# Optimization experiments

Hardware: AMD Instinct MI355X
Metric: run time of the kernel (lower is better)

## Reference

```python
import jax, jax.numpy as jnp
import numpy as np

KERNELS = (7, 9, 11)   # kernel_sizes, dilation=1 each
HEADS_PER = 2          # num_head // len(kernel_sizes)
HEAD_DIM = 32          # dim // num_head
DIM = 192


def _win_idx(L, K):
    # NATTEN non-causal window start: centered, clamped to stay in-bounds.
    starts = jnp.clip(jnp.arange(L) - K // 2, 0, L - K)
    return starts[:, None] + jnp.arange(K)[None, :]  # [L, K]


def _na2d(q, k, v, K):
    # q,k,v: [B, h, H, W, D]; q pre-scaled. Neighborhood attention, kernel KxK.
    B, h, H, W, D = q.shape
    ih = _win_idx(H, K)  # [H, K]
    iw = _win_idx(W, K)  # [W, K]
    kr = k[:, :, ih]     # [B, h, H, Kh, W, D]  rows gathered once
    # loop over the Kw kernel taps (small fixed structural loop)
    attn = jnp.stack(
        [jnp.einsum('bnijd,bnikjd->bnijk', q, kr[:, :, :, :, iw[:, kw], :])
         for kw in range(K)], axis=-1)                 # [B,h,H,W,Kh,Kw]
    attn = jax.nn.softmax(attn.reshape(B, h, H, W, K * K), axis=-1)
    attn = attn.reshape(B, h, H, W, K, K)
    vr = v[:, :, ih]     # [B, h, H, Kh, W, D]
    y = jnp.zeros_like(q)
    for kw in range(K):
        y = y + jnp.einsum('bnijk,bnikjd->bnijd',
                           attn[..., kw], vr[:, :, :, :, iw[:, kw], :])
    return y             # [B, h, H, W, D]


def _forward(x, w_qkv, b_qkv, w_proj, b_proj):
    B, H, W, C = x.shape
    qkv = x @ w_qkv + b_qkv                      # [B,H,W,3*DIM]
    scale = HEAD_DIM ** -0.5
    outs = []
    off = 0
    for K in KERNELS:
        ch = 3 * HEADS_PER * HEAD_DIM            # 192 per scale
        xi = qkv[..., off:off + ch]
        off += ch
        r = xi.reshape(B, H, W, 3, HEADS_PER, HEAD_DIM)
        q = jnp.transpose(r[:, :, :, 0], (0, 3, 1, 2, 4)) * scale
        k = jnp.transpose(r[:, :, :, 1], (0, 3, 1, 2, 4))
        v = jnp.transpose(r[:, :, :, 2], (0, 3, 1, 2, 4))
        y = _na2d(q, k, v, K)                    # [B,h,H,W,D]
        outs.append(jnp.transpose(y, (0, 2, 3, 1, 4)).reshape(B, H, W, HEADS_PER * HEAD_DIM))
    out = jnp.concatenate(outs, axis=-1)         # [B,H,W,DIM]
    return out @ w_proj + b_proj


def setup_inputs() -> dict:
    key = jax.random.key(0)
    ks = jax.random.split(key, 4)
    x = jax.random.normal(ks[0], (4, 96, 96, DIM), jnp.float32)
    w_qkv = jax.random.normal(ks[1], (DIM, 3 * DIM), jnp.float32) * 0.02
    b_qkv = jnp.zeros((3 * DIM,), jnp.float32)
    w_proj = jax.random.normal(ks[2], (DIM, DIM), jnp.float32) * 0.02
    b_proj = jnp.zeros((DIM,), jnp.float32)
    return {'x': x, 'w_qkv': w_qkv, 'b_qkv': b_qkv, 'w_proj': w_proj, 'b_proj': b_proj}


def reference(x, w_qkv, b_qkv, w_proj, b_proj):
    return _forward(x, w_qkv, b_qkv, w_proj, b_proj)
```

## Files before the change

### kernel.cpp

```cpp
#include <hip/hip_runtime.h>
#include <cstddef>

constexpr int B_ = 4, H_ = 96, W_ = 96, C_ = 192, QKVC = 576;
constexpr int NPIX = B_ * H_ * W_;
constexpr float C2 = 0.25503486208385085f;

typedef __attribute__((ext_vector_type(8))) short bf16x8;
typedef __attribute__((ext_vector_type(4))) float f32x4;
typedef unsigned short ushort_t;

__device__ __forceinline__ unsigned short f2bf(float f) {
    unsigned int u = __builtin_bit_cast(unsigned int, f);
    u += 0x7fffu + ((u >> 16) & 1u);
    return (unsigned short)(u >> 16);
}
__device__ __forceinline__ float bf2f(unsigned short h) {
    unsigned int u = ((unsigned int)h) << 16;
    return __builtin_bit_cast(float, u);
}
__device__ __forceinline__ unsigned int pack2(unsigned short a, unsigned short b) {
    return (unsigned int)a | ((unsigned int)b << 16);
}
__device__ __forceinline__ float fexp2(float x) {
#if __has_builtin(__builtin_amdgcn_exp2f)
    return __builtin_amdgcn_exp2f(x);
#else
    return __expf(x * 0.6931471805599453f);
#endif
}

__global__ __launch_bounds__(256) void convert_x_kernel(
    const float* __restrict__ x, ushort_t* __restrict__ xh, int n4)
{
    int i = blockIdx.x * 256 + threadIdx.x;
    if (i >= n4) return;
    float4 v = ((const float4*)x)[i];
    uint2 p;
    p.x = pack2(f2bf(v.x), f2bf(v.y));
    p.y = pack2(f2bf(v.z), f2bf(v.w));
    ((uint2*)xh)[i] = p;
}

__global__ __launch_bounds__(256) void convert_w_kernel(
    const float* __restrict__ w_qkv, const float* __restrict__ w_proj,
    ushort_t* __restrict__ wqt, ushort_t* __restrict__ wpt_h,
    ushort_t* __restrict__ wpt_l)
{
    int idx = blockIdx.x * 256 + threadIdx.x;
    if (idx < 576 * 192) {
        int n = idx / 192, k = idx - n * 192;
        wqt[idx] = f2bf(w_qkv[(size_t)k * 576 + n]);
    } else {
        int i2 = idx - 576 * 192;
        if (i2 < 192 * 192) {
            int n = i2 / 192, k = i2 - n * 192;
            float v = w_proj[(size_t)k * 192 + n];
            unsigned short h = f2bf(v);
            wpt_h[i2] = h;
            wpt_l[i2] = f2bf(v - bf2f(h));
        }
    }
}

template<bool BSPLIT, bool OUTBF, bool VT, int NT>
__global__ __launch_bounds__(256) void gemm_mfma2_kernel(
    const ushort_t* __restrict__ A,
    const ushort_t* __restrict__ Bt_h, const ushort_t* __restrict__ Bt_l,
    const float* __restrict__ bias, void* __restrict__ Cout,
    ushort_t* __restrict__ vTout, int M, int N, int K)
{
    constexpr int NPB = BSPLIT ? 2 : 1;
    constexpr int NI = NT / 32;
    __shared__ __align__(16) ushort_t As[8 * 64 * 8];
    __shared__ __align__(16) ushort_t Bs[NPB][8 * NT * 8];

    const int tid = threadIdx.x;
    const int lane = tid & 63;
    const int w = tid >> 6;
    const int wm = (w & 1) * 32;
    const int wn = (w >> 1) * (NT / 2);
    const int fm = lane & 15;
    const int fq = lane >> 4;

    const int phys = blockIdx.x;
    const int bid = (phys & 7) * (int)(gridDim.x >> 3) + (phys >> 3);
    const int ntiles = N / NT;
    const int m0 = (bid / ntiles) * 64;
    const int n0 = (bid % ntiles) * NT;

    f32x4 acc[2][NI];
    #pragma unroll
    for (int mi = 0; mi < 2; ++mi)
        #pragma unroll
        for (int ni = 0; ni < NI; ++ni)
            acc[mi][ni] = (f32x4){0.f, 0.f, 0.f, 0.f};

    for (int k0 = 0; k0 < K; k0 += 64) {
        __syncthreads();
        #pragma unroll
        for (int it = 0; it < 2; ++it) {
            int idx = it * 256 + tid;
            int m = idx >> 3, kc = idx & 7;
            uint4 v = *(const uint4*)(A + (size_t)(m0 + m) * K + k0 + kc * 8);
            *(uint4*)(&As[0] + (kc * 64 + (m ^ kc)) * 8) = v;
        }
        #pragma unroll
        for (int it = 0; it < NI; ++it) {
            int idx = it * 256 + tid;
            int n = idx >> 3, kc = idx & 7;
            int phys_g = kc * NT + (n ^ kc);
            *(uint4*)(&Bs[0][0] + phys_g * 8) =
                *(const uint4*)(Bt_h + (size_t)(n0 + n) * K + k0 + kc * 8);
            if constexpr (BSPLIT)
                *(uint4*)(&Bs[NPB - 1][0] + phys_g * 8) =
                    *(const uint4*)(Bt_l + (size_t)(n0 + n) * K + k0 + kc * 8);
        }
        __syncthreads();

        #pragma unroll
        for (int kt2 = 0; kt2 < 2; ++kt2) {
            const int kc = kt2 * 4 + fq;
            bf16x8 ah[2], bh[NI];
            #pragma unroll
            for (int mi = 0; mi < 2; ++mi)
                ah[mi] = *(const bf16x8*)(&As[0] + (kc * 64 + ((wm + mi * 16 + fm) ^ kc)) * 8);
            #pragma unroll
            for (int ni = 0; ni < NI; ++ni)
                bh[ni] = *(const bf16x8*)(&Bs[0][0] + (kc * NT + ((wn + ni * 16 + fm) ^ kc)) * 8);
            #pragma unroll
            for (int mi = 0; mi < 2; ++mi)
                #pragma unroll
                for (int ni = 0; ni < NI; ++ni)
                    acc[mi][ni] = __builtin_amdgcn_mfma_f32_16x16x32_bf16(
                        ah[mi], bh[ni], acc[mi][ni], 0, 0, 0);
            if constexpr (BSPLIT) {
                bf16x8 bl[NI];
                #pragma unroll
                for (int ni = 0; ni < NI; ++ni)
                    bl[ni] = *(const bf16x8*)(&Bs[NPB - 1][0] + (kc * NT + ((wn + ni * 16 + fm) ^ kc)) * 8);
                #pragma unroll
                for (int mi = 0; mi < 2; ++mi)
                    #pragma unroll
                    for (int ni = 0; ni < NI; ++ni)
                        acc[mi][ni] = __builtin_amdgcn_mfma_f32_16x16x32_bf16(
                            ah[mi], bl[ni], acc[mi][ni], 0, 0, 0);
            }
        }
    }

    #pragma unroll
    for (int ni = 0; ni < NI; ++ni) {
        const int lcol = wn + ni * 16 + fm;
        const int col = n0 + lcol;
        const float bv = bias[col];
        const int vl = lcol - 128;
        #pragma unroll
        for (int mi = 0; mi < 2; ++mi) {
            const int rbase = m0 + wm + mi * 16 + fq * 4;
            if constexpr (VT) {
                if (vl >= 0) {
                    int bb = rbase / 9216;
                    int rem = rbase - bb * 9216;
                    int ii = rem / 96;
                    int jj = rem - ii * 96;
                    int hh = vl >> 5, dd = vl & 31;
                    unsigned long long pk =
                          (unsigned long long)f2bf(acc[mi][ni][0] + bv)
                        | ((unsigned long long)f2bf(acc[mi][ni][1] + bv) << 16)
                        | ((unsigned long long)f2bf(acc[mi][ni][2] + bv) << 32)
                        | ((unsigned long long)f2bf(acc[mi][ni][3] + bv) << 48);
                    *(unsigned long long*)(vTout
                        + ((size_t)((bb * 96 + ii) * 6) + (n0 / 192) * 2 + hh) * 3072
                        + (size_t)dd * 96 + jj) = pk;
                    continue;
                }
            }
            #pragma unroll
            for (int r = 0; r < 4; ++r) {
                float val = acc[mi][ni][r] + bv;
                if constexpr (OUTBF)
                    ((ushort_t*)Cout)[(size_t)(rbase + r) * N + col] = f2bf(val);
                else
                    ((float*)Cout)[(size_t)(rbase + r) * N + col] = val;
            }
        }
    }
}

__global__ __launch_bounds__(384, 5) void na2d_kernel(
    const ushort_t* __restrict__ qkv, const ushort_t* __restrict__ vT,
    ushort_t* __restrict__ attn)
{
    __shared__ ushort_t Kb[2][96 * 40];
    __shared__ ushort_t Vtb[2][32 * 104];

    int phys = blockIdx.x;
    int idx = (phys & 7) * 288 + (phys >> 3);

    const int g = idx % 3; idx /= 3;
    const int h = idx & 1; idx >>= 1;
    const int i = idx % 96;
    const int b = idx / 96;

    const int K = 7 + 2 * g, cc = K >> 1;
    int si = i - cc; if (si < 0) si = 0; if (si > H_ - K) si = H_ - K;

    const int tid = threadIdx.x;
    const int w = tid >> 6, lane = tid & 63;
    const int fm = lane & 15, fq = lane >> 4;
    const int pixbase = w * 16;

    int cb = (pixbase - cc) & ~7;
    if (cb < 0) cb = 0; if (cb > 64) cb = 64;
    const int col0 = cb + fm, col1 = cb + 16 + fm;

    const int jlane = pixbase + fm;
    int sjl = jlane - cc; if (sjl < 0) sjl = 0; if (sjl > W_ - K) sjl = W_ - K;
    float b0[4], b1[4];
    #pragma unroll
    for (int r = 0; r < 4; ++r) {
        b0[r] = ((unsigned)(cb + fq * 4 + r - sjl)      < (unsigned)K) ? 0.f : -1e30f;
        b1[r] = ((unsigned)(cb + 16 + fq * 4 + r - sjl) < (unsigned)K) ? 0.f : -1e30f;
    }

    const size_t rowstride = (size_t)W_ * QKVC;
    const bf16x8 qfrag = *(const bf16x8*)(
        qkv + (size_t)(b * H_ + i) * rowstride + (size_t)jlane * QKVC
        + g * 192 + h * 32 + fq * 8);

    const int scol = tid >> 2, sch = tid & 3;
    const size_t kgoff = (size_t)scol * QKVC + g * 192 + 64 + h * 32 + sch * 8;
    const int klds = scol * 40 + ((sch ^ (scol & 3)) << 3);
    const int vd = tid / 12, vc8 = tid - vd * 12;
    const int vlds = vd * 104 + vc8 * 8;
    const size_t vslice = ((size_t)((b * H_ + si) * 6) + g * 2 + h) * 3072;

    f32x4 y0 = {0.f, 0.f, 0.f, 0.f}, y1 = {0.f, 0.f, 0.f, 0.f};
    float lsum = 0.f;

    uint4 kv = *(const uint4*)(qkv + (size_t)(b * H_ + si) * rowstride + kgoff);
    uint4 vv = *(const uint4*)(vT + vslice + (size_t)tid * 8);

    for (int t = 0; t < K; ++t) {
        *(uint4*)&Kb[t & 1][klds] = kv;
        *(uint4*)&Vtb[t & 1][vlds] = vv;
        if (t + 1 < K) {
            kv = *(const uint4*)(qkv + (size_t)(b * H_ + si + t + 1) * rowstride + kgoff);
            vv = *(const uint4*)(vT + vslice + (size_t)(t + 1) * 18432 + (size_t)tid * 8);
        }
        __syncthreads();

        bf16x8 kf0 = *(const bf16x8*)&Kb[t & 1][col0 * 40 + ((fq ^ (col0 & 3)) << 3)];
        bf16x8 kf1 = *(const bf16x8*)&Kb[t & 1][col1 * 40 + ((fq ^ (col1 & 3)) << 3)];
        const ushort_t* vb0 = &Vtb[t & 1][fm * 104 + cb + fq * 4];
        const ushort_t* vb1 = &Vtb[t & 1][(16 + fm) * 104 + cb + fq * 4];
        uint2 va0 = *(const uint2*)(vb0);
        uint2 va1 = *(const uint2*)(vb0 + 16);
        uint2 va2 = *(const uint2*)(vb1);
        uint2 va3 = *(const uint2*)(vb1 + 16);
        const bf16x8 cv0 = __builtin_bit_cast(bf16x8, (uint4){va0.x, va0.y, va1.x, va1.y});
        const bf16x8 cv1 = __builtin_bit_cast(bf16x8, (uint4){va2.x, va2.y, va3.x, va3.y});

        f32x4 s0 = __builtin_amdgcn_mfma_f32_16x16x32_bf16(
            kf0, qfrag, (f32x4){0.f, 0.f, 0.f, 0.f}, 0, 0, 0);
        f32x4 s1 = __builtin_amdgcn_mfma_f32_16x16x32_bf16(
            kf1, qfrag, (f32x4){0.f, 0.f, 0.f, 0.f}, 0, 0, 0);

        unsigned short p00 = f2bf(fexp2(fmaf(s0[0], C2, b0[0])));
        unsigned short p01 = f2bf(fexp2(fmaf(s0[1], C2, b0[1])));
        unsigned short p02 = f2bf(fexp2(fmaf(s0[2], C2, b0[2])));
        unsigned short p03 = f2bf(fexp2(fmaf(s0[3], C2, b0[3])));
        unsigned short p10 = f2bf(fexp2(fmaf(s1[0], C2, b1[0])));
        unsigned short p11 = f2bf(fexp2(fmaf(s1[1], C2, b1[1])));
        unsigned short p12 = f2bf(fexp2(fmaf(s1[2], C2, b1[2])));
        unsigned short p13 = f2bf(fexp2(fmaf(s1[3], C2, b1[3])));
        lsum += (bf2f(p00) + bf2f(p01)) + (bf2f(p02) + bf2f(p03))
              + (bf2f(p10) + bf2f(p11)) + (bf2f(p12) + bf2f(p13));
        const bf16x8 pa = __builtin_bit_cast(bf16x8, (uint4){
            pack2(p00, p01), pack2(p02, p03),
            pack2(p10, p11), pack2(p12, p13)});

        y0 = __builtin_amdgcn_mfma_f32_16x16x32_bf16(pa, cv0, y0, 0, 0, 0);
        y1 = __builtin_amdgcn_mfma_f32_16x16x32_bf16(pa, cv1, y1, 0, 0, 0);
    }

    lsum += __shfl_xor(lsum, 16);
    lsum += __shfl_xor(lsum, 32);

    #pragma unroll
    for (int r = 0; r < 4; ++r) {
        const float l = __shfl(lsum, fq * 4 + r);
        const float inv = 1.f / l;
        const int j = pixbase + fq * 4 + r;
        const size_t o = (size_t)((b * H_ + i) * W_ + j) * C_ + g * 64 + h * 32 + fm;
        attn[o]      = f2bf(y0[r] * inv);
        attn[o + 16] = f2bf(y1[r] * inv);
    }
}

extern "C" void kernel_launch(void* const* d_in, const int* in_sizes, int n_in,
                              void* d_out, int out_size, void* d_ws, size_t ws_size,
                              hipStream_t stream)
{
    const float* x      = (const float*)d_in[0];
    const float* w_qkv  = (const float*)d_in[1];
    const float* b_qkv  = (const float*)d_in[2];
    const float* w_proj = (const float*)d_in[3];
    const float* b_proj = (const float*)d_in[4];
    float* out = (float*)d_out;

    char* ws = (char*)d_ws;
    ushort_t* qkvh  = (ushort_t*)ws;
    char*     reg1  = ws + (size_t)NPIX * QKVC * 2;
    ushort_t* xh    = (ushort_t*)reg1;
    ushort_t* attn  = (ushort_t*)reg1;
    char*     wbase = reg1 + (size_t)NPIX * C_ * 2;
    ushort_t* wqt   = (ushort_t*)wbase;
    ushort_t* wpt_h = (ushort_t*)(wbase + 576 * 192 * 2);
    ushort_t* wpt_l = (ushort_t*)(wbase + 576 * 192 * 2 + 192 * 192 * 2);
    ushort_t* vT    = (ushort_t*)(wbase + 576 * 192 * 2 + 2 * 192 * 192 * 2);

    convert_x_kernel<<<(NPIX * C_ / 4 + 255) / 256, 256, 0, stream>>>(
        x, xh, NPIX * C_ / 4);
    convert_w_kernel<<<(576 * 192 + 192 * 192 + 255) / 256, 256, 0, stream>>>(
        w_qkv, w_proj, wqt, wpt_h, wpt_l);

    gemm_mfma2_kernel<false, true, true, 192><<<(NPIX / 64) * (QKVC / 192), 256, 0, stream>>>(
        xh, wqt, nullptr, b_qkv, qkvh, vT, NPIX, QKVC, C_);

    na2d_kernel<<<2304, 384, 0, stream>>>(qkvh, vT, attn);

    gemm_mfma2_kernel<true, false, false, 96><<<(NPIX / 64) * (C_ / 96), 256, 0, stream>>>(
        attn, wpt_h, wpt_l, b_proj, out, nullptr, NPIX, C_, C_);
}
```

Measured before the change: 155.5 us.

## Fuse x fp32-to-bf16 conversion into QKV GEMM and register-prefetch next K tile

The separate kernel that converts x to bf16 is removed. The QKV GEMM now reads fp32 x directly and packs it to bf16 while writing shared memory, which saves one launch and a full write and re-read of a bf16 copy of x. The GEMM main loop is also restructured so the next K tile's global loads are issued into registers before the MFMA work on the current tile, overlapping memory latency with compute. In exchange the kernel uses more registers, and the QKV GEMM reads twice as many A bytes because x is now fp32. Since x is converted three times (once per N tile), the fp32 reads are repeated.

```diff
diff --git a/kernel.cpp b/kernel.cpp
--- a/kernel.cpp
+++ b/kernel.cpp
@@ -27,18 +27,6 @@
 #else
     return __expf(x * 0.6931471805599453f);
 #endif
-}
-
-__global__ __launch_bounds__(256) void convert_x_kernel(
-    const float* __restrict__ x, ushort_t* __restrict__ xh, int n4)
-{
-    int i = blockIdx.x * 256 + threadIdx.x;
-    if (i >= n4) return;
-    float4 v = ((const float4*)x)[i];
-    uint2 p;
-    p.x = pack2(f2bf(v.x), f2bf(v.y));
-    p.y = pack2(f2bf(v.z), f2bf(v.w));
-    ((uint2*)xh)[i] = p;
 }
 
 __global__ __launch_bounds__(256) void convert_w_kernel(
@@ -62,9 +50,9 @@
     }
 }
 
-template<bool BSPLIT, bool OUTBF, bool VT, int NT>
+template<bool BSPLIT, bool OUTBF, bool VT, int NT, bool AF32>
 __global__ __launch_bounds__(256) void gemm_mfma2_kernel(
-    const ushort_t* __restrict__ A,
+    const void* __restrict__ Ain,
     const ushort_t* __restrict__ Bt_h, const ushort_t* __restrict__ Bt_l,
     const float* __restrict__ bias, void* __restrict__ Cout,
     ushort_t* __restrict__ vTout, int M, int N, int K)
@@ -88,6 +76,9 @@
     const int m0 = (bid / ntiles) * 64;
     const int n0 = (bid % ntiles) * NT;
 
+    const int sa_m  = (tid >> 3);
+    const int sa_kc = tid & 7;
+
     f32x4 acc[2][NI];
     #pragma unroll
     for (int mi = 0; mi < 2; ++mi)
@@ -95,26 +86,63 @@
         for (int ni = 0; ni < NI; ++ni)
             acc[mi][ni] = (f32x4){0.f, 0.f, 0.f, 0.f};
 
-    for (int k0 = 0; k0 < K; k0 += 64) {
-        __syncthreads();
+    float4 af[2][2];
+    uint4  au[2];
+    uint4  bu[NI];
+    uint4  blu[BSPLIT ? NI : 1];
+
+    const int NS = K / 64;
+
+    auto stage = [&](int k0) {
         #pragma unroll
         for (int it = 0; it < 2; ++it) {
-            int idx = it * 256 + tid;
-            int m = idx >> 3, kc = idx & 7;
-            uint4 v = *(const uint4*)(A + (size_t)(m0 + m) * K + k0 + kc * 8);
-            *(uint4*)(&As[0] + (kc * 64 + (m ^ kc)) * 8) = v;
+            const int m = sa_m + it * 32;
+            if constexpr (AF32) {
+                const float* ap = (const float*)Ain + (size_t)(m0 + m) * K + k0 + sa_kc * 8;
+                af[it][0] = *(const float4*)(ap);
+                af[it][1] = *(const float4*)(ap + 4);
+            } else {
+                au[it] = *(const uint4*)((const ushort_t*)Ain
+                    + (size_t)(m0 + m) * K + k0 + sa_kc * 8);
+            }
         }
         #pragma unroll
         for (int it = 0; it < NI; ++it) {
-            int idx = it * 256 + tid;
-            int n = idx >> 3, kc = idx & 7;
-            int phys_g = kc * NT + (n ^ kc);
-            *(uint4*)(&Bs[0][0] + phys_g * 8) =
-                *(const uint4*)(Bt_h + (size_t)(n0 + n) * K + k0 + kc * 8);
+            const int n = sa_m + it * 32;
+            bu[it] = *(const uint4*)(Bt_h + (size_t)(n0 + n) * K + k0 + sa_kc * 8);
             if constexpr (BSPLIT)
-                *(uint4*)(&Bs[NPB - 1][0] + phys_g * 8) =
-                    *(const uint4*)(Bt_l + (size_t)(n0 + n) * K + k0 + kc * 8);
-        }
+                blu[it] = *(const uint4*)(Bt_l + (size_t)(n0 + n) * K + k0 + sa_kc * 8);
+        }
+    };
+    auto commit = [&]() {
+        #pragma unroll
+        for (int it = 0; it < 2; ++it) {
+            const int m = sa_m + it * 32;
+            uint4 v;
+            if constexpr (AF32) {
+                v.x = pack2(f2bf(af[it][0].x), f2bf(af[it][0].y));
+                v.y = pack2(f2bf(af[it][0].z), f2bf(af[it][0].w));
+                v.z = pack2(f2bf(af[it][1].x), f2bf(af[it][1].y));
+                v.w = pack2(f2bf(af[it][1].z), f2bf(af[it][1].w));
+            } else {
+                v = au[it];
+            }
+            *(uint4*)(&As[0] + (sa_kc * 64 + (m ^ sa_kc)) * 8) = v;
+        }
+        #pragma unroll
+        for (int it = 0; it < NI; ++it) {
+            const int n = sa_m + it * 32;
+            const int phys_g = sa_kc * NT + (n ^ sa_kc);
+            *(uint4*)(&Bs[0][0] + phys_g * 8) = bu[it];
+            if constexpr (BSPLIT)
+                *(uint4*)(&Bs[NPB - 1][0] + phys_g * 8) = blu[it];
+        }
+    };
+
+    stage(0);
+    for (int s = 0; s < NS; ++s) {
+        commit();
+        if (s + 1 < NS) stage((s + 1) * 64);
         __syncthreads();
 
         #pragma unroll
@@ -146,6 +174,7 @@
                             ah[mi], bl[ni], acc[mi][ni], 0, 0, 0);
             }
         }
+        if (s + 1 < NS) __syncthreads();
     }
 
     #pragma unroll
@@ -312,7 +341,6 @@
     char* ws = (char*)d_ws;
     ushort_t* qkvh  = (ushort_t*)ws;
     char*     reg1  = ws + (size_t)NPIX * QKVC * 2;
-    ushort_t* xh    = (ushort_t*)reg1;
     ushort_t* attn  = (ushort_t*)reg1;
     char*     wbase = reg1 + (size_t)NPIX * C_ * 2;
     ushort_t* wqt   = (ushort_t*)wbase;
@@ -320,16 +348,14 @@
     ushort_t* wpt_l = (ushort_t*)(wbase + 576 * 192 * 2 + 192 * 192 * 2);
     ushort_t* vT    = (ushort_t*)(wbase + 576 * 192 * 2 + 2 * 192 * 192 * 2);
 
-    convert_x_kernel<<<(NPIX * C_ / 4 + 255) / 256, 256, 0, stream>>>(
-        x, xh, NPIX * C_ / 4);
     convert_w_kernel<<<(576 * 192 + 192 * 192 + 255) / 256, 256, 0, stream>>>(
         w_qkv, w_proj, wqt, wpt_h, wpt_l);
 
-    gemm_mfma2_kernel<false, true, true, 192><<<(NPIX / 64) * (QKVC / 192), 256, 0, stream>>>(
-        xh, wqt, nullptr, b_qkv, qkvh, vT, NPIX, QKVC, C_);
+    gemm_mfma2_kernel<false, true, true, 192, true><<<(NPIX / 64) * (QKVC / 192), 256, 0, stream>>>(
+        x, wqt, nullptr, b_qkv, qkvh, vT, NPIX, QKVC, C_);
 
     na2d_kernel<<<2304, 384, 0, stream>>>(qkvh, vT, attn);
 
-    gemm_mfma2_kernel<true, false, false, 96><<<(NPIX / 64) * (C_ / 96), 256, 0, stream>>>(
+    gemm_mfma2_kernel<true, false, false, 96, false><<<(NPIX / 64) * (C_ / 96), 256, 0, stream>>>(
         attn, wpt_h, wpt_l, b_proj, out, nullptr, NPIX, C_, C_);
 }
```

Result: slower. 214.4 us (+37.9%).

## Fuse x bf16 conversion into QKV GEMM and coalesce V-transpose stores via LDS

Applied to the files above, without the earlier changes.

Removes the standalone fp32-to-bf16 conversion kernel for x and converts A tiles on the fly inside the QKV GEMM load. This avoids one launch and a full write and read of the bf16 copy of x. Each N-tile block now reads fp32 x, so x is fetched redundantly across the three column tiles. The V-transposed output is also staged through shared memory so global stores become 16-byte contiguous chunks instead of scattered 8-byte writes.

```diff
diff --git a/kernel.cpp b/kernel.cpp
--- a/kernel.cpp
+++ b/kernel.cpp
@@ -27,18 +27,6 @@
 #else
     return __expf(x * 0.6931471805599453f);
 #endif
-}
-
-__global__ __launch_bounds__(256) void convert_x_kernel(
-    const float* __restrict__ x, ushort_t* __restrict__ xh, int n4)
-{
-    int i = blockIdx.x * 256 + threadIdx.x;
-    if (i >= n4) return;
-    float4 v = ((const float4*)x)[i];
-    uint2 p;
-    p.x = pack2(f2bf(v.x), f2bf(v.y));
-    p.y = pack2(f2bf(v.z), f2bf(v.w));
-    ((uint2*)xh)[i] = p;
 }
 
 __global__ __launch_bounds__(256) void convert_w_kernel(
@@ -62,9 +50,9 @@
     }
 }
 
-template<bool BSPLIT, bool OUTBF, bool VT, int NT>
+template<bool BSPLIT, bool OUTBF, bool VT, int NT, bool AF32>
 __global__ __launch_bounds__(256) void gemm_mfma2_kernel(
-    const ushort_t* __restrict__ A,
+    const void* __restrict__ Ain,
     const ushort_t* __restrict__ Bt_h, const ushort_t* __restrict__ Bt_l,
     const float* __restrict__ bias, void* __restrict__ Cout,
     ushort_t* __restrict__ vTout, int M, int N, int K)
@@ -101,7 +89,19 @@
         for (int it = 0; it < 2; ++it) {
             int idx = it * 256 + tid;
             int m = idx >> 3, kc = idx & 7;
-            uint4 v = *(const uint4*)(A + (size_t)(m0 + m) * K + k0 + kc * 8);
+            uint4 v;
+            if constexpr (AF32) {
+                const float* ap = (const float*)Ain + (size_t)(m0 + m) * K + k0 + kc * 8;
+                float4 a0 = *(const float4*)(ap);
+                float4 a1 = *(const float4*)(ap + 4);
+                v.x = pack2(f2bf(a0.x), f2bf(a0.y));
+                v.y = pack2(f2bf(a0.z), f2bf(a0.w));
+                v.z = pack2(f2bf(a1.x), f2bf(a1.y));
+                v.w = pack2(f2bf(a1.z), f2bf(a1.w));
+            } else {
+                v = *(const uint4*)((const ushort_t*)Ain
+                    + (size_t)(m0 + m) * K + k0 + kc * 8);
+            }
             *(uint4*)(&As[0] + (kc * 64 + (m ^ kc)) * 8) = v;
         }
         #pragma unroll
@@ -152,29 +152,12 @@
     for (int ni = 0; ni < NI; ++ni) {
         const int lcol = wn + ni * 16 + fm;
         const int col = n0 + lcol;
+        const int vl = lcol - 128;
+        if (VT && vl >= 0) continue;
         const float bv = bias[col];
-        const int vl = lcol - 128;
         #pragma unroll
         for (int mi = 0; mi < 2; ++mi) {
             const int rbase = m0 + wm + mi * 16 + fq * 4;
-            if constexpr (VT) {
-                if (vl >= 0) {
-                    int bb = rbase / 9216;
-                    int rem = rbase - bb * 9216;
-                    int ii = rem / 96;
-                    int jj = rem - ii * 96;
-                    int hh = vl >> 5, dd = vl & 31;
-                    unsigned long long pk =
-                          (unsigned long long)f2bf(acc[mi][ni][0] + bv)
-                        | ((unsigned long long)f2bf(acc[mi][ni][1] + bv) << 16)
-                        | ((unsigned long long)f2bf(acc[mi][ni][2] + bv) << 32)
-                        | ((unsigned long long)f2bf(acc[mi][ni][3] + bv) << 48);
-                    *(unsigned long long*)(vTout
-                        + ((size_t)((bb * 96 + ii) * 6) + (n0 / 192) * 2 + hh) * 3072
-                        + (size_t)dd * 96 + jj) = pk;
-                    continue;
-                }
-            }
             #pragma unroll
             for (int r = 0; r < 4; ++r) {
                 float val = acc[mi][ni][r] + bv;
@@ -184,6 +167,43 @@
                     ((float*)Cout)[(size_t)(rbase + r) * N + col] = val;
             }
         }
+    }
+
+    if constexpr (VT) {
+        ushort_t* Vst = &Bs[0][0];
+        __syncthreads();
+        if (w >= 2) {
+            #pragma unroll
+            for (int ni = 2; ni < NI; ++ni) {
+                const int vcol = (ni - 2) * 16 + fm;
+                const float bv = bias[n0 + 128 + vcol];
+                #pragma unroll
+                for (int mi = 0; mi < 2; ++mi) {
+                    const int rowb = wm + mi * 16 + fq * 4;
+                    unsigned long long pk =
+                          (unsigned long long)f2bf(acc[mi][ni][0] + bv)
+                        | ((unsigned long long)f2bf(acc[mi][ni][1] + bv) << 16)
+                        | ((unsigned long long)f2bf(acc[mi][ni][2] + bv) << 32)
+                        | ((unsigned long long)f2bf(acc[mi][ni][3] + bv) << 48);
+                    *(unsigned long long*)&Vst[vcol * 72 + rowb] = pk;
+                }
+            }
+        }
+        __syncthreads();
+        const int vcol = tid >> 2;
+        const int rowb = (tid & 3) * 16;
+        uint4 q0 = *(const uint4*)&Vst[vcol * 72 + rowb];
+        uint4 q1 = *(const uint4*)&Vst[vcol * 72 + rowb + 8];
+        const int pix = m0 + rowb;
+        const int bb = pix / 9216;
+        const int rem = pix - bb * 9216;
+        const int ii = rem / 96;
+        const int jj = rem - ii * 96;
+        ushort_t* dst = vTout
+            + ((size_t)((bb * 96 + ii) * 6) + (n0 / 192) * 2 + (vcol >> 5)) * 3072
+            + (size_t)(vcol & 31) * 96 + jj;
+        *(uint4*)dst = q0;
+        *(uint4*)(dst + 8) = q1;
     }
 }
 
@@ -312,7 +332,6 @@
     char* ws = (char*)d_ws;
     ushort_t* qkvh  = (ushort_t*)ws;
     char*     reg1  = ws + (size_t)NPIX * QKVC * 2;
-    ushort_t* xh    = (ushort_t*)reg1;
     ushort_t* attn  = (ushort_t*)reg1;
     char*     wbase = reg1 + (size_t)NPIX * C_ * 2;
     ushort_t* wqt   = (ushort_t*)wbase;
@@ -320,16 +339,14 @@
     ushort_t* wpt_l = (ushort_t*)(wbase + 576 * 192 * 2 + 192 * 192 * 2);
     ushort_t* vT    = (ushort_t*)(wbase + 576 * 192 * 2 + 2 * 192 * 192 * 2);
 
-    convert_x_kernel<<<(NPIX * C_ / 4 + 255) / 256, 256, 0, stream>>>(
-        x, xh, NPIX * C_ / 4);
     convert_w_kernel<<<(576 * 192 + 192 * 192 + 255) / 256, 256, 0, stream>>>(
         w_qkv, w_proj, wqt, wpt_h, wpt_l);
 
-    gemm_mfma2_kernel<false, true, true, 192><<<(NPIX / 64) * (QKVC / 192), 256, 0, stream>>>(
-        xh, wqt, nullptr, b_qkv, qkvh, vT, NPIX, QKVC, C_);
+    gemm_mfma2_kernel<false, true, true, 192, true><<<(NPIX / 64) * (QKVC / 192), 256, 0, stream>>>(
+        x, wqt, nullptr, b_qkv, qkvh, vT, NPIX, QKVC, C_);
 
     na2d_kernel<<<2304, 384, 0, stream>>>(qkvh, vT, attn);
 
-    gemm_mfma2_kernel<true, false, false, 96><<<(NPIX / 64) * (C_ / 96), 256, 0, stream>>>(
+    gemm_mfma2_kernel<true, false, false, 96, false><<<(NPIX / 64) * (C_ / 96), 256, 0, stream>>>(
         attn, wpt_h, wpt_l, b_proj, out, nullptr, NPIX, C_, C_);
 }
```

Result: slower. 161.0 us (+3.6%).

## Process two query rows per NA2D block and merge conversion kernels

Applied to the files above, without the earlier changes.

Each neighborhood-attention block now handles two adjacent query rows. It loads the union of their key/value windows once, which is K+1 rows at most, and computes both rows' attention from the same LDS tiles. This roughly halves K/V global traffic and barrier count per output row, and the grid is halved. The x and weight conversion kernels are also merged into one launch to save a launch. The cost is more registers for the second set of accumulators, fewer blocks in flight, and divergent per-row masking of iterations.

```diff
diff --git a/kernel.cpp b/kernel.cpp
--- a/kernel.cpp
+++ b/kernel.cpp
@@ -29,24 +29,22 @@
 #endif
 }
 
-__global__ __launch_bounds__(256) void convert_x_kernel(
-    const float* __restrict__ x, ushort_t* __restrict__ xh, int n4)
+__global__ __launch_bounds__(256) void convert_all_kernel(
+    const float* __restrict__ x, const float* __restrict__ w_qkv,
+    const float* __restrict__ w_proj,
+    ushort_t* __restrict__ xh, ushort_t* __restrict__ wqt,
+    ushort_t* __restrict__ wpt_h, ushort_t* __restrict__ wpt_l, int n4)
 {
     int i = blockIdx.x * 256 + threadIdx.x;
-    if (i >= n4) return;
-    float4 v = ((const float4*)x)[i];
-    uint2 p;
-    p.x = pack2(f2bf(v.x), f2bf(v.y));
-    p.y = pack2(f2bf(v.z), f2bf(v.w));
-    ((uint2*)xh)[i] = p;
-}
-
-__global__ __launch_bounds__(256) void convert_w_kernel(
-    const float* __restrict__ w_qkv, const float* __restrict__ w_proj,
-    ushort_t* __restrict__ wqt, ushort_t* __restrict__ wpt_h,
-    ushort_t* __restrict__ wpt_l)
-{
-    int idx = blockIdx.x * 256 + threadIdx.x;
+    if (i < n4) {
+        float4 v = ((const float4*)x)[i];
+        uint2 p;
+        p.x = pack2(f2bf(v.x), f2bf(v.y));
+        p.y = pack2(f2bf(v.z), f2bf(v.w));
+        ((uint2*)xh)[i] = p;
+        return;
+    }
+    int idx = i - n4;
     if (idx < 576 * 192) {
         int n = idx / 192, k = idx - n * 192;
         wqt[idx] = f2bf(w_qkv[(size_t)k * 576 + n]);
@@ -195,15 +193,19 @@
     __shared__ ushort_t Vtb[2][32 * 104];
 
     int phys = blockIdx.x;
-    int idx = (phys & 7) * 288 + (phys >> 3);
+    int idx = (phys & 7) * 144 + (phys >> 3);
 
     const int g = idx % 3; idx /= 3;
     const int h = idx & 1; idx >>= 1;
-    const int i = idx % 96;
-    const int b = idx / 96;
+    const int R = idx % 48;
+    const int b = idx / 48;
+    const int i0 = R * 2, i1 = i0 + 1;
 
     const int K = 7 + 2 * g, cc = K >> 1;
-    int si = i - cc; if (si < 0) si = 0; if (si > H_ - K) si = H_ - K;
+    int si0 = i0 - cc; if (si0 < 0) si0 = 0; if (si0 > H_ - K) si0 = H_ - K;
+    int si1 = i1 - cc; if (si1 < 0) si1 = 0; if (si1 > H_ - K) si1 = H_ - K;
+    const int off1 = si1 - si0;
+    const int NTr = K + off1;
 
     const int tid = threadIdx.x;
     const int w = tid >> 6, lane = tid & 63;
@@ -224,48 +226,27 @@
     }
 
     const size_t rowstride = (size_t)W_ * QKVC;
-    const bf16x8 qfrag = *(const bf16x8*)(
-        qkv + (size_t)(b * H_ + i) * rowstride + (size_t)jlane * QKVC
-        + g * 192 + h * 32 + fq * 8);
+    const size_t qoff = (size_t)jlane * QKVC + g * 192 + h * 32 + fq * 8;
+    const bf16x8 qfragA = *(const bf16x8*)(qkv + (size_t)(b * H_ + i0) * rowstride + qoff);
+    const bf16x8 qfragB = *(const bf16x8*)(qkv + (size_t)(b * H_ + i1) * rowstride + qoff);
 
     const int scol = tid >> 2, sch = tid & 3;
     const size_t kgoff = (size_t)scol * QKVC + g * 192 + 64 + h * 32 + sch * 8;
     const int klds = scol * 40 + ((sch ^ (scol & 3)) << 3);
     const int vd = tid / 12, vc8 = tid - vd * 12;
     const int vlds = vd * 104 + vc8 * 8;
-    const size_t vslice = ((size_t)((b * H_ + si) * 6) + g * 2 + h) * 3072;
-
-    f32x4 y0 = {0.f, 0.f, 0.f, 0.f}, y1 = {0.f, 0.f, 0.f, 0.f};
-    float lsum = 0.f;
-
-    uint4 kv = *(const uint4*)(qkv + (size_t)(b * H_ + si) * rowstride + kgoff);
+    const size_t vslice = ((size_t)((b * H_ + si0) * 6) + g * 2 + h) * 3072;
+
+    f32x4 ya0 = {0.f,0.f,0.f,0.f}, ya1 = {0.f,0.f,0.f,0.f};
+    f32x4 yb0 = {0.f,0.f,0.f,0.f}, yb1 = {0.f,0.f,0.f,0.f};
+    float lsumA = 0.f, lsumB = 0.f;
+
+    uint4 kv = *(const uint4*)(qkv + (size_t)(b * H_ + si0) * rowstride + kgoff);
     uint4 vv = *(const uint4*)(vT + vslice + (size_t)tid * 8);
 
-    for (int t = 0; t < K; ++t) {
-        *(uint4*)&Kb[t & 1][klds] = kv;
-        *(uint4*)&Vtb[t & 1][vlds] = vv;
-        if (t + 1 < K) {
-            kv = *(const uint4*)(qkv + (size_t)(b * H_ + si + t + 1) * rowstride + kgoff);
-            vv = *(const uint4*)(vT + vslice + (size_t)(t + 1) * 18432 + (size_t)tid * 8);
-        }
-        __syncthreads();
-
-        bf16x8 kf0 = *(const bf16x8*)&Kb[t & 1][col0 * 40 + ((fq ^ (col0 & 3)) << 3)];
-        bf16x8 kf1 = *(const bf16x8*)&Kb[t & 1][col1 * 40 + ((fq ^ (col1 & 3)) << 3)];
-        const ushort_t* vb0 = &Vtb[t & 1][fm * 104 + cb + fq * 4];
-        const ushort_t* vb1 = &Vtb[t & 1][(16 + fm) * 104 + cb + fq * 4];
-        uint2 va0 = *(const uint2*)(vb0);
-        uint2 va1 = *(const uint2*)(vb0 + 16);
-        uint2 va2 = *(const uint2*)(vb1);
-        uint2 va3 = *(const uint2*)(vb1 + 16);
-        const bf16x8 cv0 = __builtin_bit_cast(bf16x8, (uint4){va0.x, va0.y, va1.x, va1.y});
-        const bf16x8 cv1 = __builtin_bit_cast(bf16x8, (uint4){va2.x, va2.y, va3.x, va3.y});
-
-        f32x4 s0 = __builtin_amdgcn_mfma_f32_16x16x32_bf16(
-            kf0, qfrag, (f32x4){0.f, 0.f, 0.f, 0.f}, 0, 0, 0);
-        f32x4 s1 = __builtin_amdgcn_mfma_f32_16x16x32_bf16(
-            kf1, qfrag, (f32x4){0.f, 0.f, 0.f, 0.f}, 0, 0, 0);
-
+    auto softmax_pv = [&](const f32x4& s0, const f32x4& s1, float& lsum,
+                          const bf16x8& cv0, const bf16x8& cv1,
+                          f32x4& y0, f32x4& y1) {
         unsigned short p00 = f2bf(fexp2(fmaf(s0[0], C2, b0[0])));
         unsigned short p01 = f2bf(fexp2(fmaf(s0[1], C2, b0[1])));
         unsigned short p02 = f2bf(fexp2(fmaf(s0[2], C2, b0[2])));
@@ -279,22 +260,63 @@
         const bf16x8 pa = __builtin_bit_cast(bf16x8, (uint4){
             pack2(p00, p01), pack2(p02, p03),
             pack2(p10, p11), pack2(p12, p13)});
-
         y0 = __builtin_amdgcn_mfma_f32_16x16x32_bf16(pa, cv0, y0, 0, 0, 0);
         y1 = __builtin_amdgcn_mfma_f32_16x16x32_bf16(pa, cv1, y1, 0, 0, 0);
-    }
-
-    lsum += __shfl_xor(lsum, 16);
-    lsum += __shfl_xor(lsum, 32);
+    };
+
+    for (int t = 0; t < NTr; ++t) {
+        *(uint4*)&Kb[t & 1][klds] = kv;
+        *(uint4*)&Vtb[t & 1][vlds] = vv;
+        if (t + 1 < NTr) {
+            kv = *(const uint4*)(qkv + (size_t)(b * H_ + si0 + t + 1) * rowstride + kgoff);
+            vv = *(const uint4*)(vT + vslice + (size_t)(t + 1) * 18432 + (size_t)tid * 8);
+        }
+        __syncthreads();
+
+        bf16x8 kf0 = *(const bf16x8*)&Kb[t & 1][col0 * 40 + ((fq ^ (col0 & 3)) << 3)];
+        bf16x8 kf1 = *(const bf16x8*)&Kb[t & 1][col1 * 40 + ((fq ^ (col1 & 3)) << 3)];
+        const ushort_t* vb0 = &Vtb[t & 1][fm * 104 + cb + fq * 4];
+        const ushort_t* vb1 = &Vtb[t & 1][(16 + fm) * 104 + cb + fq * 4];
+        uint2 va0 = *(const uint2*)(vb0);
+        uint2 va1 = *(const uint2*)(vb0 + 16);
+        uint2 va2 = *(const uint2*)(vb1);
+        uint2 va3 = *(const uint2*)(vb1 + 16);
+        const bf16x8 cv0 = __builtin_bit_cast(bf16x8, (uint4){va0.x, va0.y, va1.x, va1.y});
+        const bf16x8 cv1 = __builtin_bit_cast(bf16x8, (uint4){va2.x, va2.y, va3.x, va3.y});
+
+        if (t < K) {
+            f32x4 s0 = __builtin_amdgcn_mfma_f32_16x16x32_bf16(
+                kf0, qfragA, (f32x4){0.f, 0.f, 0.f, 0.f}, 0, 0, 0);
+            f32x4 s1 = __builtin_amdgcn_mfma_f32_16x16x32_bf16(
+                kf1, qfragA, (f32x4){0.f, 0.f, 0.f, 0.f}, 0, 0, 0);
+            softmax_pv(s0, s1, lsumA, cv0, cv1, ya0, ya1);
+        }
+        if (t >= off1) {
+            f32x4 s0 = __builtin_amdgcn_mfma_f32_16x16x32_bf16(
+                kf0, qfragB, (f32x4){0.f, 0.f, 0.f, 0.f}, 0, 0, 0);
+            f32x4 s1 = __builtin_amdgcn_mfma_f32_16x16x32_bf16(
+                kf1, qfragB, (f32x4){0.f, 0.f, 0.f, 0.f}, 0, 0, 0);
+            softmax_pv(s0, s1, lsumB, cv0, cv1, yb0, yb1);
+        }
+    }
+
+    lsumA += __shfl_xor(lsumA, 16);
+    lsumA += __shfl_xor(lsumA, 32);
+    lsumB += __shfl_xor(lsumB, 16);
+    lsumB += __shfl_xor(lsumB, 32);
 
     #pragma unroll
     for (int r = 0; r < 4; ++r) {
-        const float l = __shfl(lsum, fq * 4 + r);
-        const float inv = 1.f / l;
         const int j = pixbase + fq * 4 + r;
-        const size_t o = (size_t)((b * H_ + i) * W_ + j) * C_ + g * 64 + h * 32 + fm;
-        attn[o]      = f2bf(y0[r] * inv);
-        attn[o + 16] = f2bf(y1[r] * inv);
+        const float lA = __shfl(lsumA, fq * 4 + r);
+        const float lB = __shfl(lsumB, fq * 4 + r);
+        const float invA = 1.f / lA, invB = 1.f / lB;
+        const size_t oA = (size_t)((b * H_ + i0) * W_ + j) * C_ + g * 64 + h * 32 + fm;
+        const size_t oB = (size_t)((b * H_ + i1) * W_ + j) * C_ + g * 64 + h * 32 + fm;
+        attn[oA]      = f2bf(ya0[r] * invA);
+        attn[oA + 16] = f2bf(ya1[r] * invA);
+        attn[oB]      = f2bf(yb0[r] * invB);
+        attn[oB + 16] = f2bf(yb1[r] * invB);
     }
 }
 
@@ -320,15 +342,13 @@
     ushort_t* wpt_l = (ushort_t*)(wbase + 576 * 192 * 2 + 192 * 192 * 2);
     ushort_t* vT    = (ushort_t*)(wbase + 576 * 192 * 2 + 2 * 192 * 192 * 2);
 
-    convert_x_kernel<<<(NPIX * C_ / 4 + 255) / 256, 256, 0, stream>>>(
-        x, xh, NPIX * C_ / 4);
-    convert_w_kernel<<<(576 * 192 + 192 * 192 + 255) / 256, 256, 0, stream>>>(
-        w_qkv, w_proj, wqt, wpt_h, wpt_l);
+    convert_all_kernel<<<7488, 256, 0, stream>>>(
+        x, w_qkv, w_proj, xh, wqt, wpt_h, wpt_l, NPIX * C_ / 4);
 
     gemm_mfma2_kernel<false, true, true, 192><<<(NPIX / 64) * (QKVC / 192), 256, 0, stream>>>(
         xh, wqt, nullptr, b_qkv, qkvh, vT, NPIX, QKVC, C_);
 
-    na2d_kernel<<<2304, 384, 0, stream>>>(qkvh, vT, attn);
+    na2d_kernel<<<1152, 384, 0, stream>>>(qkvh, vT, attn);
 
     gemm_mfma2_kernel<true, false, false, 96><<<(NPIX / 64) * (C_ / 96), 256, 0, stream>>>(
         attn, wpt_h, wpt_l, b_proj, out, nullptr, NPIX, C_, C_);
```

Result: no change. 155.7 us (+0.2%).
